# Kernel optimization log

Hardware: AMD Instinct MI355X
Metric: run time of the kernel (lower is better)

## Reference

```python
import jax, jax.numpy as jnp
import numpy as np

N_AGENTS = 16          # args.n_agents
B = 262144             # batch size
D = 16                 # num_test (encoder output dim)
H = 32                 # num_units (hidden dim)
LN_EPS = 1e-5
SCALE = np.float32(1.0 / np.sqrt(D))


def _mlp(x, W1, b1, W2, b2):
    # Linear->ReLU->Linear->ReLU encoder
    h = jax.nn.relu(x @ W1 + b1)
    return jax.nn.relu(h @ W2 + b2)


def _ln_relu(x, g, b):
    # nn.LayerNorm(D) followed by ReLU
    mu = jnp.mean(x, axis=-1, keepdims=True)
    var = jnp.var(x, axis=-1, keepdims=True)
    return jax.nn.relu((x - mu) * jax.lax.rsqrt(var + LN_EPS) * g + b)


def setup_inputs() -> dict:
    key = jax.random.key(0)
    ks = jax.random.split(key, 11)
    def lin(k, i, o):
        return (jax.random.normal(k, (i, o), jnp.float32) / np.sqrt(i)).astype(jnp.float32)
    n = N_AGENTS
    in_dim = 4 + (n - 1) * 4 + n * 2  # 96
    return {
        "s_input": jax.random.normal(ks[0], (B, in_dim), jnp.float32),
        "en_W1": lin(ks[1], 4, H), "en_b1": jnp.zeros((H,), jnp.float32),
        "en_W2": lin(ks[2], H, D), "en_b2": jnp.zeros((D,), jnp.float32),
        "oa_W1": lin(ks[3], 4, H), "oa_b1": jnp.zeros((H,), jnp.float32),
        "oa_W2": lin(ks[4], H, D), "oa_b2": jnp.zeros((D,), jnp.float32),
        "goal_W1": lin(ks[5], 2, H), "goal_b1": jnp.zeros((H,), jnp.float32),
        "goal_W2": lin(ks[6], H, D), "goal_b2": jnp.zeros((D,), jnp.float32),
        "oa_ln_g": jnp.ones((D,), jnp.float32), "oa_ln_b": jnp.zeros((D,), jnp.float32),
        "goal_ln_g": jnp.ones((D,), jnp.float32), "goal_ln_b": jnp.zeros((D,), jnp.float32),
        "act_W1": lin(ks[7], 3 * D, H), "act_b1": jnp.zeros((H,), jnp.float32),
        "act_W2": lin(ks[8], H, H), "act_b2": jnp.zeros((H,), jnp.float32),
        "act_W3": lin(ks[9], H, 2), "act_b3": jnp.zeros((2,), jnp.float32),
    }


def reference(s_input, en_W1, en_b1, en_W2, en_b2,
              oa_W1, oa_b1, oa_W2, oa_b2,
              goal_W1, goal_b1, goal_W2, goal_b2,
              oa_ln_g, oa_ln_b, goal_ln_g, goal_ln_b,
              act_W1, act_b1, act_W2, act_b2, act_W3, act_b3):
    n = N_AGENTS
    K = n - 1
    bsz = s_input.shape[0]

    # self encoder: [B,4] -> [B,D]
    self_out = _mlp(s_input[:, :4], en_W1, en_b1, en_W2, en_b2)

    # other agents: layout is (n-1)*2 positions then (n-1)*2 velocities,
    # regrouped per-agent into [B,K,4] (vectorizes the per-i stacking loop)
    og = s_input[:, 4:4 + K * 4]
    other_in = jnp.concatenate(
        [og[:, :K * 2].reshape(bsz, K, 2), og[:, K * 2:].reshape(bsz, K, 2)],
        axis=-1)  # [B,K,4]
    other_enc = _mlp(other_in, oa_W1, oa_b1, oa_W2, oa_b2)  # [B,K,D]

    def attend(enc):
        # scaled-dot attention of self_out against encoded neighbors/goals
        scores = jnp.einsum('bd,bkd->bk', self_out, enc) * SCALE
        attn = jax.nn.softmax(scores, axis=-1)
        return jnp.einsum('bk,bkd->bd', attn, enc)  # [B,D]

    other_pool = _ln_relu(attend(other_enc), oa_ln_g, oa_ln_b)

    # goals: last n*2 cols split into n chunks of 2 -> [B,n,2]
    food_in = s_input[:, -n * 2:].reshape(bsz, n, 2)
    food_enc = _mlp(food_in, goal_W1, goal_b1, goal_W2, goal_b2)  # [B,n,D]
    food_pool = _ln_relu(attend(food_enc), goal_ln_g, goal_ln_b)

    # merge order matches torch.cat([self_out, food_out, other_good_out], 1)
    merged = jnp.concatenate([self_out, food_pool, other_pool], axis=1)  # [B,3D]
    h = jax.nn.leaky_relu(merged @ act_W1 + act_b1)  # slope 0.01 (torch default)
    h = jax.nn.leaky_relu(h @ act_W2 + act_b2)
    return jnp.tanh(h @ act_W3 + act_b3)  # [B,2]
```

## Files before the change

### kernel.cpp

```cpp
#include <hip/hip_runtime.h>
#include <stdint.h>


#define LN_EPS 1e-5f

typedef _Float16 h2 __attribute__((ext_vector_type(2)));

struct Weights {
  const float* __restrict__ en_W1; const float* __restrict__ en_b1;
  const float* __restrict__ en_W2; const float* __restrict__ en_b2;
  const float* __restrict__ oa_W1; const float* __restrict__ oa_b1;
  const float* __restrict__ oa_W2; const float* __restrict__ oa_b2;
  const float* __restrict__ go_W1; const float* __restrict__ go_b1;
  const float* __restrict__ go_W2; const float* __restrict__ go_b2;
  const float* __restrict__ oa_g;  const float* __restrict__ oa_b;
  const float* __restrict__ go_g;  const float* __restrict__ go_b;
  const float* __restrict__ a_W1;  const float* __restrict__ a_b1;
  const float* __restrict__ a_W2;  const float* __restrict__ a_b2;
  const float* __restrict__ a_W3;  const float* __restrict__ a_b3;
};

constexpr int P_EN_W1 = 0;
constexpr int P_EN_W2 = 64;
constexpr int P_OA_W1 = 320;
constexpr int P_OA_W2 = 384;
constexpr int P_GO_W1 = 640;
constexpr int P_GO_W2 = 672;
constexpr int P_A_W1  = 928;
constexpr int P_A_W2  = 1696;
constexpr int P_A_W3  = 2208;

__device__ __forceinline__ float2 ld2(const float* __restrict__ p) {
  return *reinterpret_cast<const float2*>(p);
}
__device__ __forceinline__ uint32_t pack_rne(float a, float b) {
  h2 v; v.x = (_Float16)a; v.y = (_Float16)b;
  return __builtin_bit_cast(uint32_t, v);
}
__device__ __forceinline__ h2 asH2(uint32_t u) { return __builtin_bit_cast(h2, u); }
__device__ __forceinline__ float fdot2(h2 a, h2 b, float c) {
  return __builtin_amdgcn_fdot2(a, b, c, false);
}
__device__ __forceinline__ h2 pkrtz(float a, float b) {
  return __builtin_bit_cast(h2, __builtin_amdgcn_cvt_pkrtz(a, b));
}

__global__ void prep_weights(Weights W, uint32_t* __restrict__ ws) {
  const int t = threadIdx.x;
  if (t < 32) {
    ws[P_EN_W1 + t]      = pack_rne(W.en_W1[t],      W.en_W1[32 + t]);
    ws[P_EN_W1 + 32 + t] = pack_rne(W.en_W1[64 + t], W.en_W1[96 + t]);
    ws[P_OA_W1 + t]      = pack_rne(W.oa_W1[t],      W.oa_W1[32 + t]);
    ws[P_OA_W1 + 32 + t] = pack_rne(W.oa_W1[64 + t], W.oa_W1[96 + t]);
    ws[P_GO_W1 + t]      = pack_rne(W.go_W1[t],      W.go_W1[32 + t]);
  }
  {
    int jp = t >> 4, d = t & 15;
    ws[P_EN_W2 + t] = pack_rne(W.en_W2[(2*jp)*16 + d], W.en_W2[(2*jp+1)*16 + d]);
    ws[P_OA_W2 + t] = pack_rne(W.oa_W2[(2*jp)*16 + d], W.oa_W2[(2*jp+1)*16 + d]);
    ws[P_GO_W2 + t] = pack_rne(W.go_W2[(2*jp)*16 + d], W.go_W2[(2*jp+1)*16 + d]);
  }
  for (int i = t; i < 768; i += 256) {
    int cp = i >> 5, j = i & 31;
    ws[P_A_W1 + i] = pack_rne(W.a_W1[(2*cp)*32 + j], W.a_W1[(2*cp+1)*32 + j]);
  }
  for (int i = t; i < 512; i += 256) {
    int cp = i >> 5, j = i & 31;
    ws[P_A_W2 + i] = pack_rne(W.a_W2[(2*cp)*32 + j], W.a_W2[(2*cp+1)*32 + j]);
  }
  if (t < 32) {
    int cp = t >> 1, o = t & 1;
    ws[P_A_W3 + t] = pack_rne(W.a_W3[(2*cp)*2 + o], W.a_W3[(2*cp+1)*2 + o]);
  }
}

template<int NE>
__device__ __forceinline__ void oa_batch(const float* __restrict__ srow, int k0,
                                         const Weights& W,
                                         const uint32_t* __restrict__ wsu,
                                         const float (&self_out)[16],
                                         float (&acc)[16], float& m, float& l) {
  h2 a01[NE], a23[NE];
#pragma unroll
  for (int e = 0; e < NE; ++e) {
    float2 x = ld2(srow + 4  + 2*(k0 + e));
    float2 y = ld2(srow + 34 + 2*(k0 + e));
    a01[e] = pkrtz(x.x, x.y);
    a23[e] = pkrtz(y.x, y.y);
  }
  float enc[NE][16];
#pragma unroll
  for (int d = 0; d < 16; ++d) {
    float b2 = W.oa_b2[d];
#pragma unroll
    for (int e = 0; e < NE; ++e) enc[e][d] = b2;
  }
#pragma unroll
  for (int jp = 0; jp < 16; ++jp) {
    const int j0 = 2*jp, j1 = 2*jp + 1;
    const float b10 = W.oa_b1[j0], b11 = W.oa_b1[j1];
    const h2 wA0 = asH2(wsu[P_OA_W1 + j0]), wB0 = asH2(wsu[P_OA_W1 + 32 + j0]);
    const h2 wA1 = asH2(wsu[P_OA_W1 + j1]), wB1 = asH2(wsu[P_OA_W1 + 32 + j1]);
    h2 hh[NE];
#pragma unroll
    for (int e = 0; e < NE; ++e) {
      float h0 = fmaxf(fdot2(a01[e], wA0, fdot2(a23[e], wB0, b10)), 0.f);
      float h1 = fmaxf(fdot2(a01[e], wA1, fdot2(a23[e], wB1, b11)), 0.f);
      hh[e] = pkrtz(h0, h1);
    }
#pragma unroll
    for (int d = 0; d < 16; ++d) {
      const h2 wd = asH2(wsu[P_OA_W2 + jp*16 + d]);
#pragma unroll
      for (int e = 0; e < NE; ++e) enc[e][d] = fdot2(hh[e], wd, enc[e][d]);
    }
  }
#pragma unroll
  for (int e = 0; e < NE; ++e) {
    float s = 0.f;
#pragma unroll
    for (int d = 0; d < 16; ++d) {
      enc[e][d] = fmaxf(enc[e][d], 0.f);
      s = fmaf(self_out[d], enc[e][d], s);
    }
    s *= 0.25f;
    float mn = fmaxf(m, s);
    float alpha = __expf(m - mn), w = __expf(s - mn);
    l = fmaf(l, alpha, w);
#pragma unroll
    for (int d = 0; d < 16; ++d) acc[d] = fmaf(acc[d], alpha, w * enc[e][d]);
    m = mn;
  }
}

template<int NE>
__device__ __forceinline__ void go_batch(const float* __restrict__ srow, int k0,
                                         const Weights& W,
                                         const uint32_t* __restrict__ wsu,
                                         const float (&self_out)[16],
                                         float (&acc)[16], float& m, float& l) {
  h2 ah[NE];
#pragma unroll
  for (int e = 0; e < NE; ++e) {
    float2 x = ld2(srow + 64 + 2*(k0 + e));
    ah[e] = pkrtz(x.x, x.y);
  }
  float enc[NE][16];
#pragma unroll
  for (int d = 0; d < 16; ++d) {
    float b2 = W.go_b2[d];
#pragma unroll
    for (int e = 0; e < NE; ++e) enc[e][d] = b2;
  }
#pragma unroll
  for (int jp = 0; jp < 16; ++jp) {
    const int j0 = 2*jp, j1 = 2*jp + 1;
    const float b10 = W.go_b1[j0], b11 = W.go_b1[j1];
    const h2 w0 = asH2(wsu[P_GO_W1 + j0]);
    const h2 w1 = asH2(wsu[P_GO_W1 + j1]);
    h2 hh[NE];
#pragma unroll
    for (int e = 0; e < NE; ++e) {
      float h0 = fmaxf(fdot2(ah[e], w0, b10), 0.f);
      float h1 = fmaxf(fdot2(ah[e], w1, b11), 0.f);
      hh[e] = pkrtz(h0, h1);
    }
#pragma unroll
    for (int d = 0; d < 16; ++d) {
      const h2 wd = asH2(wsu[P_GO_W2 + jp*16 + d]);
#pragma unroll
      for (int e = 0; e < NE; ++e) enc[e][d] = fdot2(hh[e], wd, enc[e][d]);
    }
  }
#pragma unroll
  for (int e = 0; e < NE; ++e) {
    float s = 0.f;
#pragma unroll
    for (int d = 0; d < 16; ++d) {
      enc[e][d] = fmaxf(enc[e][d], 0.f);
      s = fmaf(self_out[d], enc[e][d], s);
    }
    s *= 0.25f;
    float mn = fmaxf(m, s);
    float alpha = __expf(m - mn), w = __expf(s - mn);
    l = fmaf(l, alpha, w);
#pragma unroll
    for (int d = 0; d < 16; ++d) acc[d] = fmaf(acc[d], alpha, w * enc[e][d]);
    m = mn;
  }
}

__global__ __launch_bounds__(256, 2)
void actor_fwd(const float* __restrict__ s_input, Weights W,
               const uint32_t* __restrict__ wsu,
               float* __restrict__ out, int bsz) {
  const int lane    = threadIdx.x & 63;
  const int wv      = threadIdx.x >> 6;
  const int pairIdx = wv >> 1;
  const int role    = wv & 1;
  int row = blockIdx.x * 128 + pairIdx * 64 + lane;
  row = min(row, bsz - 1);
  const float* __restrict__ srow = s_input + (size_t)row * 96;

  __shared__ float fpool[2][64][17];

  float self_out[16];
  {
    float2 p01 = ld2(srow + 0);
    float2 p23 = ld2(srow + 2);
    h2 a01 = pkrtz(p01.x, p01.y);
    h2 a23 = pkrtz(p23.x, p23.y);
#pragma unroll
    for (int d = 0; d < 16; ++d) self_out[d] = W.en_b2[d];
#pragma unroll
    for (int jp = 0; jp < 16; ++jp) {
      const int j0 = 2*jp, j1 = 2*jp + 1;
      float h0 = fmaxf(fdot2(a01, asH2(wsu[P_EN_W1 + j0]),
                     fdot2(a23, asH2(wsu[P_EN_W1 + 32 + j0]), W.en_b1[j0])), 0.f);
      float h1 = fmaxf(fdot2(a01, asH2(wsu[P_EN_W1 + j1]),
                     fdot2(a23, asH2(wsu[P_EN_W1 + 32 + j1]), W.en_b1[j1])), 0.f);
      h2 hh = pkrtz(h0, h1);
#pragma unroll
      for (int d = 0; d < 16; ++d)
        self_out[d] = fdot2(hh, asH2(wsu[P_EN_W2 + jp*16 + d]), self_out[d]);
    }
#pragma unroll
    for (int d = 0; d < 16; ++d) self_out[d] = fmaxf(self_out[d], 0.f);
  }

  float other_pool[16];

  if (role == 0) {
    float m = -3.0e38f, l = 0.f, acc[16];
#pragma unroll
    for (int d = 0; d < 16; ++d) acc[d] = 0.f;
#pragma unroll 1
    for (int k0 = 0; k0 < 15; k0 += 3)
      oa_batch<3>(srow, k0, W, wsu, self_out, acc, m, l);

    float inv = 1.f / l;
    float mu = 0.f;
#pragma unroll
    for (int d = 0; d < 16; ++d) { acc[d] *= inv; mu += acc[d]; }
    mu *= (1.f / 16.f);
    float var = 0.f;
#pragma unroll
    for (int d = 0; d < 16; ++d) { float x = acc[d] - mu; var = fmaf(x, x, var); }
    var *= (1.f / 16.f);
    float rstd = rsqrtf(var + LN_EPS);
#pragma unroll
    for (int d = 0; d < 16; ++d)
      other_pool[d] = fmaxf(fmaf((acc[d] - mu) * rstd, W.oa_g[d], W.oa_b[d]), 0.f);
  } else {
    float m = -3.0e38f, l = 0.f, acc[16];
#pragma unroll
    for (int d = 0; d < 16; ++d) acc[d] = 0.f;
#pragma unroll 1
    for (int k0 = 0; k0 < 16; k0 += 4)
      go_batch<4>(srow, k0, W, wsu, self_out, acc, m, l);

    float inv = 1.f / l;
    float mu = 0.f;
#pragma unroll
    for (int d = 0; d < 16; ++d) { acc[d] *= inv; mu += acc[d]; }
    mu *= (1.f / 16.f);
    float var = 0.f;
#pragma unroll
    for (int d = 0; d < 16; ++d) { float x = acc[d] - mu; var = fmaf(x, x, var); }
    var *= (1.f / 16.f);
    float rstd = rsqrtf(var + LN_EPS);
#pragma unroll
    for (int d = 0; d < 16; ++d) {
      float fp = fmaxf(fmaf((acc[d] - mu) * rstd, W.go_g[d], W.go_b[d]), 0.f);
      fpool[pairIdx][lane][d] = fp;
    }
  }

  __syncthreads();
  if (role != 0) return;

  float food_pool[16];
#pragma unroll
  for (int d = 0; d < 16; ++d) food_pool[d] = fpool[pairIdx][lane][d];

  h2 mh[24];
#pragma unroll
  for (int c = 0; c < 8; ++c) mh[c]      = pkrtz(self_out[2*c],  self_out[2*c+1]);
#pragma unroll
  for (int c = 0; c < 8; ++c) mh[8 + c]  = pkrtz(food_pool[2*c], food_pool[2*c+1]);
#pragma unroll
  for (int c = 0; c < 8; ++c) mh[16 + c] = pkrtz(other_pool[2*c], other_pool[2*c+1]);

  float h1v[32];
#pragma unroll
  for (int j = 0; j < 32; ++j) h1v[j] = W.a_b1[j];
#pragma unroll
  for (int cp = 0; cp < 24; ++cp) {
    h2 v = mh[cp];
#pragma unroll
    for (int j = 0; j < 32; ++j)
      h1v[j] = fdot2(v, asH2(wsu[P_A_W1 + cp*32 + j]), h1v[j]);
  }
#pragma unroll
  for (int j = 0; j < 32; ++j) h1v[j] = fmaxf(h1v[j], 0.01f * h1v[j]);

  h2 hh1[16];
#pragma unroll
  for (int c = 0; c < 16; ++c) hh1[c] = pkrtz(h1v[2*c], h1v[2*c+1]);

  float h2v[32];
#pragma unroll
  for (int j = 0; j < 32; ++j) h2v[j] = W.a_b2[j];
#pragma unroll
  for (int cp = 0; cp < 16; ++cp) {
    h2 v = hh1[cp];
#pragma unroll
    for (int j = 0; j < 32; ++j)
      h2v[j] = fdot2(v, asH2(wsu[P_A_W2 + cp*32 + j]), h2v[j]);
  }
#pragma unroll
  for (int j = 0; j < 32; ++j) h2v[j] = fmaxf(h2v[j], 0.01f * h2v[j]);

  h2 hh2[16];
#pragma unroll
  for (int c = 0; c < 16; ++c) hh2[c] = pkrtz(h2v[2*c], h2v[2*c+1]);

  float o0 = W.a_b3[0], o1 = W.a_b3[1];
#pragma unroll
  for (int cp = 0; cp < 16; ++cp) {
    o0 = fdot2(hh2[cp], asH2(wsu[P_A_W3 + cp*2 + 0]), o0);
    o1 = fdot2(hh2[cp], asH2(wsu[P_A_W3 + cp*2 + 1]), o1);
  }
  o0 = tanhf(o0);
  o1 = tanhf(o1);

  reinterpret_cast<float2*>(out)[row] = make_float2(o0, o1);
}

extern "C" void kernel_launch(void* const* d_in, const int* in_sizes, int n_in,
                              void* d_out, int out_size, void* d_ws, size_t ws_size,
                              hipStream_t stream) {
  const float* s_input = (const float*)d_in[0];
  Weights W;
  W.en_W1 = (const float*)d_in[1];  W.en_b1 = (const float*)d_in[2];
  W.en_W2 = (const float*)d_in[3];  W.en_b2 = (const float*)d_in[4];
  W.oa_W1 = (const float*)d_in[5];  W.oa_b1 = (const float*)d_in[6];
  W.oa_W2 = (const float*)d_in[7];  W.oa_b2 = (const float*)d_in[8];
  W.go_W1 = (const float*)d_in[9];  W.go_b1 = (const float*)d_in[10];
  W.go_W2 = (const float*)d_in[11]; W.go_b2 = (const float*)d_in[12];
  W.oa_g  = (const float*)d_in[13]; W.oa_b  = (const float*)d_in[14];
  W.go_g  = (const float*)d_in[15]; W.go_b  = (const float*)d_in[16];
  W.a_W1  = (const float*)d_in[17]; W.a_b1  = (const float*)d_in[18];
  W.a_W2  = (const float*)d_in[19]; W.a_b2  = (const float*)d_in[20];
  W.a_W3  = (const float*)d_in[21]; W.a_b3  = (const float*)d_in[22];

  uint32_t* wsu = (uint32_t*)d_ws;
  prep_weights<<<1, 256, 0, stream>>>(W, wsu);

  const int bsz = in_sizes[0] / 96;
  const int blocks = (bsz + 127) / 128;
  actor_fwd<<<blocks, 256, 0, stream>>>(s_input, W, wsu, (float*)d_out, bsz);
}
```

Before: 316.6 us.

## Cut register pressure: pack self_out to half2, smaller batches, higher occupancy

Keeps the self encoder output as 8 packed half2 values instead of 16 floats, and computes the attention score with fdot2 on packed halves. Shrinks the per-batch neighbor and goal batches to 2 (plus a tail of 1 for the 15 others), and raises the launch-bounds minimum blocks per CU from 2 to 8. Together these aim to lower VGPR use so more waves can hide memory latency. The cost is less ILP per wave, possible spills under the tighter register cap, and slightly lower score precision from fp16 rounding.

```diff
diff --git a/kernel.cpp b/kernel.cpp
--- a/kernel.cpp
+++ b/kernel.cpp
@@ -78,7 +78,7 @@
 __device__ __forceinline__ void oa_batch(const float* __restrict__ srow, int k0,
                                          const Weights& W,
                                          const uint32_t* __restrict__ wsu,
-                                         const float (&self_out)[16],
+                                         const h2 (&selfh)[8],
                                          float (&acc)[16], float& m, float& l) {
   h2 a01[NE], a23[NE];
 #pragma unroll
@@ -119,9 +119,10 @@
   for (int e = 0; e < NE; ++e) {
     float s = 0.f;
 #pragma unroll
-    for (int d = 0; d < 16; ++d) {
-      enc[e][d] = fmaxf(enc[e][d], 0.f);
-      s = fmaf(self_out[d], enc[e][d], s);
+    for (int c = 0; c < 8; ++c) {
+      enc[e][2*c]   = fmaxf(enc[e][2*c],   0.f);
+      enc[e][2*c+1] = fmaxf(enc[e][2*c+1], 0.f);
+      s = fdot2(selfh[c], pkrtz(enc[e][2*c], enc[e][2*c+1]), s);
     }
     s *= 0.25f;
     float mn = fmaxf(m, s);
@@ -137,7 +138,7 @@
 __device__ __forceinline__ void go_batch(const float* __restrict__ srow, int k0,
                                          const Weights& W,
                                          const uint32_t* __restrict__ wsu,
-                                         const float (&self_out)[16],
+                                         const h2 (&selfh)[8],
                                          float (&acc)[16], float& m, float& l) {
   h2 ah[NE];
 #pragma unroll
@@ -176,9 +177,10 @@
   for (int e = 0; e < NE; ++e) {
     float s = 0.f;
 #pragma unroll
-    for (int d = 0; d < 16; ++d) {
-      enc[e][d] = fmaxf(enc[e][d], 0.f);
-      s = fmaf(self_out[d], enc[e][d], s);
+    for (int c = 0; c < 8; ++c) {
+      enc[e][2*c]   = fmaxf(enc[e][2*c],   0.f);
+      enc[e][2*c+1] = fmaxf(enc[e][2*c+1], 0.f);
+      s = fdot2(selfh[c], pkrtz(enc[e][2*c], enc[e][2*c+1]), s);
     }
     s *= 0.25f;
     float mn = fmaxf(m, s);
@@ -190,7 +192,7 @@
   }
 }
 
-__global__ __launch_bounds__(256, 2)
+__global__ __launch_bounds__(256, 8)
 void actor_fwd(const float* __restrict__ s_input, Weights W,
                const uint32_t* __restrict__ wsu,
                float* __restrict__ out, int bsz) {
@@ -204,12 +206,13 @@
 
   __shared__ float fpool[2][64][17];
 
-  float self_out[16];
+  h2 selfh[8];
   {
     float2 p01 = ld2(srow + 0);
     float2 p23 = ld2(srow + 2);
     h2 a01 = pkrtz(p01.x, p01.y);
     h2 a23 = pkrtz(p23.x, p23.y);
+    float self_out[16];
 #pragma unroll
     for (int d = 0; d < 16; ++d) self_out[d] = W.en_b2[d];
 #pragma unroll
@@ -225,7 +228,8 @@
         self_out[d] = fdot2(hh, asH2(wsu[P_EN_W2 + jp*16 + d]), self_out[d]);
     }
 #pragma unroll
-    for (int d = 0; d < 16; ++d) self_out[d] = fmaxf(self_out[d], 0.f);
+    for (int c = 0; c < 8; ++c)
+      selfh[c] = pkrtz(fmaxf(self_out[2*c], 0.f), fmaxf(self_out[2*c+1], 0.f));
   }
 
   float other_pool[16];
@@ -235,8 +239,9 @@
 #pragma unroll
     for (int d = 0; d < 16; ++d) acc[d] = 0.f;
 #pragma unroll 1
-    for (int k0 = 0; k0 < 15; k0 += 3)
-      oa_batch<3>(srow, k0, W, wsu, self_out, acc, m, l);
+    for (int k0 = 0; k0 < 14; k0 += 2)
+      oa_batch<2>(srow, k0, W, wsu, selfh, acc, m, l);
+    oa_batch<1>(srow, 14, W, wsu, selfh, acc, m, l);
 
     float inv = 1.f / l;
     float mu = 0.f;
@@ -256,8 +261,8 @@
 #pragma unroll
     for (int d = 0; d < 16; ++d) acc[d] = 0.f;
 #pragma unroll 1
-    for (int k0 = 0; k0 < 16; k0 += 4)
-      go_batch<4>(srow, k0, W, wsu, self_out, acc, m, l);
+    for (int k0 = 0; k0 < 16; k0 += 2)
+      go_batch<2>(srow, k0, W, wsu, selfh, acc, m, l);
 
     float inv = 1.f / l;
     float mu = 0.f;
@@ -279,15 +284,14 @@
   __syncthreads();
   if (role != 0) return;
 
-  float food_pool[16];
-#pragma unroll
-  for (int d = 0; d < 16; ++d) food_pool[d] = fpool[pairIdx][lane][d];
-
   h2 mh[24];
 #pragma unroll
-  for (int c = 0; c < 8; ++c) mh[c]      = pkrtz(self_out[2*c],  self_out[2*c+1]);
-#pragma unroll
-  for (int c = 0; c < 8; ++c) mh[8 + c]  = pkrtz(food_pool[2*c], food_pool[2*c+1]);
+  for (int c = 0; c < 8; ++c) mh[c] = selfh[c];
+#pragma unroll
+  for (int c = 0; c < 8; ++c) {
+    float f0 = fpool[pairIdx][lane][2*c], f1 = fpool[pairIdx][lane][2*c+1];
+    mh[8 + c] = pkrtz(f0, f1);
+  }
 #pragma unroll
   for (int c = 0; c < 8; ++c) mh[16 + c] = pkrtz(other_pool[2*c], other_pool[2*c+1]);
 
```

New measurement: 509.1 us. 60.8% more time.
